# Kernel tuning notes

Measured on AMD Instinct MI355X. Metric: run time of the kernel, lower is better.

## Reference

```python
import jax, jax.numpy as jnp
import numpy as np

L = 4096
NUM_ITERS = 50
LR = 0.1
B1, B2, EPS = 0.9, 0.999, 1e-8  # torch.optim.Adam defaults


def setup_inputs() -> dict:
    key = jax.random.key(0)
    k1, k2 = jax.random.split(key)
    pred_distances = jax.random.uniform(k1, (L, L), dtype=jnp.float32) * 30.0
    confidence = jax.random.uniform(k2, (L, L), dtype=jnp.float32)
    mask = jnp.ones((L, L), dtype=jnp.float32)
    return {"pred_distances": pred_distances, "confidence": confidence, "mask": mask}


def _mds_init(distances, mask):
    # Classical MDS: double-centered squared distances -> top-3 eigenpairs.
    n = distances.shape[0]
    D = jnp.where(mask == 0, 0.0, distances)
    D_sq = D ** 2
    H = jnp.eye(n, dtype=distances.dtype) - jnp.ones((n, n), dtype=distances.dtype) / n
    B = -0.5 * (H @ D_sq @ H)
    evals, evecs = jnp.linalg.eigh(B)  # ascending order
    top_evals = evals[-1:-4:-1]        # top 3, descending
    top_evecs = evecs[:, -1:-4:-1]
    return top_evecs * jnp.sqrt(jnp.clip(top_evals, 1e-10))  # (L, 3)


def _loss(coords, pred_d, weight):
    diff = coords[None, :, :] - coords[:, None, :]              # (L, L, 3)
    dist = jnp.sqrt((diff ** 2).sum(-1) + 1e-8)                 # (L, L)
    loss = (weight * (dist - pred_d) ** 2).sum() / (weight.sum() + 1e-8)
    # chain regularizer: consecutive residues ~5.9 Angstrom apart (L > 2)
    nd = jnp.sqrt(((coords[1:] - coords[:-1]) ** 2).sum(-1) + 1e-8)
    return loss + 0.1 * ((nd - 5.9) ** 2).mean()


def reference(pred_distances, confidence, mask):
    pred_d = (pred_distances + pred_distances.T) / 2
    conf = (confidence + confidence.T) / 2
    weight = conf * mask
    coords0 = _mds_init(pred_d, mask)
    grad_fn = jax.grad(_loss)

    def step(i, carry):
        coords, m, v = carry
        g = grad_fn(coords, pred_d, weight)
        t = (i + 1).astype(jnp.float32)
        m = B1 * m + (1.0 - B1) * g
        v = B2 * v + (1.0 - B2) * g * g
        mhat = m / (1.0 - B1 ** t)
        vhat = v / (1.0 - B2 ** t)
        coords = coords - LR * mhat / (jnp.sqrt(vhat) + EPS)
        return (coords, m, v)

    z = jnp.zeros_like(coords0)
    coords, _, _ = jax.lax.fori_loop(0, NUM_ITERS, step, (coords0, z, z))
    return jax.lax.stop_gradient(coords)  # torch returns coords.detach()
```

## Files before the change

kernel.cpp:

```cpp
#include <hip/hip_runtime.h>
#include <math.h>

#define SIGN0 (1.0)
#define SIGN1 (-1.0)
#define SIGN2 (1.0)
#define EMIT0 1
#define EMIT1 1
#define EMIT2 1

#define N 4096
#define M_LAN 180
#define NCOLS (M_LAN + 2)
#define TPB 256
#define TPB_G 512

__global__ void k_zerof(float* p, int n) {
  int i = blockIdx.x * blockDim.x + threadIdx.x;
  int stride = gridDim.x * blockDim.x;
  for (; i < n; i += stride) p[i] = 0.0f;
}
__global__ void k_sentinel(float* out, int n) {
  int i = blockIdx.x * blockDim.x + threadIdx.x;
  if (i < n) out[i] = 1.0e6f;
}

#define TILE 64
__global__ void k_prep(const float* __restrict__ P, const float* __restrict__ C,
                       const float* __restrict__ Mk, float* __restrict__ pd,
                       float* __restrict__ wgt, double* __restrict__ wpart) {
  __shared__ float As[TILE][TILE + 1];
  __shared__ float Bs[TILE][TILE + 1];
  __shared__ double sred[4];
  int i0 = blockIdx.x * TILE, j0 = blockIdx.y * TILE;
  int tx = threadIdx.x & 63, ty = threadIdx.x >> 6;
  float mreg[16];
  for (int rr = ty, q = 0; rr < TILE; rr += 4, ++q)
    mreg[q] = Mk[(size_t)(i0 + rr) * N + j0 + tx];
  for (int rr = ty; rr < TILE; rr += 4) {
    As[rr][tx] = P[(size_t)(i0 + rr) * N + j0 + tx];
    Bs[rr][tx] = P[(size_t)(j0 + rr) * N + i0 + tx];
  }
  __syncthreads();
  for (int rr = ty, q = 0; rr < TILE; rr += 4, ++q) {
    float pv = 0.5f * (As[rr][tx] + Bs[tx][rr]);
    pd[(size_t)(i0 + rr) * N + j0 + tx] = (mreg[q] == 0.0f) ? 0.0f : pv;
  }
  __syncthreads();
  for (int rr = ty; rr < TILE; rr += 4) {
    As[rr][tx] = C[(size_t)(i0 + rr) * N + j0 + tx];
    Bs[rr][tx] = C[(size_t)(j0 + rr) * N + i0 + tx];
  }
  __syncthreads();
  double wacc = 0.0;
  for (int rr = ty, q = 0; rr < TILE; rr += 4, ++q) {
    float wvv = 0.5f * (As[rr][tx] + Bs[tx][rr]) * mreg[q];
    wgt[(size_t)(i0 + rr) * N + j0 + tx] = wvv;
    wacc += (double)wvv;
  }
  for (int s = 32; s > 0; s >>= 1) wacc += __shfl_down(wacc, s);
  int lane = threadIdx.x & 63, wid = threadIdx.x >> 6;
  if (lane == 0) sred[wid] = wacc;
  __syncthreads();
  if (threadIdx.x == 0)
    wpart[blockIdx.y * 64 + blockIdx.x] = sred[0] + sred[1] + sred[2] + sred[3];
}

__global__ void k_wsum(const double* __restrict__ wpart, double* __restrict__ Wsum) {
  __shared__ double sred[4];
  double a = 0.0;
  for (int t = threadIdx.x; t < 4096; t += TPB) a += wpart[t];
  for (int s = 32; s > 0; s >>= 1) a += __shfl_down(a, s);
  int lane = threadIdx.x & 63, wid = threadIdx.x >> 6;
  if (lane == 0) sred[wid] = a;
  __syncthreads();
  if (threadIdx.x == 0) Wsum[0] = sred[0] + sred[1] + sred[2] + sred[3];
}

__global__ void k_init_raw(double* __restrict__ V, double* __restrict__ wv,
                           double* __restrict__ statp) {
  __shared__ double sred[4];
  int i = blockIdx.x * TPB + threadIdx.x;
  V[i] = 1.0 / 64.0;
  unsigned h = (unsigned)i * 2654435761u;
  h ^= h >> 16; h *= 2246822519u; h ^= h >> 13; h *= 3266489917u; h ^= h >> 16;
  double r = ((double)(h & 0xFFFFFFu) / 16777216.0) - 0.5;
  wv[i] = r;
  double s1 = r;
  for (int s = 32; s > 0; s >>= 1) s1 += __shfl_down(s1, s);
  int lane = threadIdx.x & 63, wid = threadIdx.x >> 6;
  if (lane == 0) sred[wid] = s1;
  __syncthreads();
  if (threadIdx.x == 0) statp[blockIdx.x] = sred[0] + sred[1] + sred[2] + sred[3];
}
__global__ void k_init_fin(double* __restrict__ wv, const double* __restrict__ statp,
                           double* __restrict__ bsqp) {
  __shared__ double sred[4];
  int i = blockIdx.x * TPB + threadIdx.x;
  double s1 = 0.0;
#pragma unroll
  for (int p = 0; p < 16; ++p) s1 += statp[p];
  double mean = s1 / (double)N;
  double w = wv[i] - mean;
  wv[i] = w;
  double ww = w * w;
  for (int s = 32; s > 0; s >>= 1) ww += __shfl_down(ww, s);
  int lane = threadIdx.x & 63, wid = threadIdx.x >> 6;
  if (lane == 0) sred[wid] = ww;
  __syncthreads();
  if (threadIdx.x == 0) bsqp[blockIdx.x] = sred[0] + sred[1] + sred[2] + sred[3];
  if (blockIdx.x == 0 && threadIdx.x >= 16 && threadIdx.x < 256) bsqp[threadIdx.x] = 0.0;
}

__global__ void __launch_bounds__(TPB) k_mv(const float* __restrict__ pd,
    const double* __restrict__ wv, double* __restrict__ V, int j,
    double* __restrict__ z, double* __restrict__ beta,
    const double* __restrict__ bsqp) {
  __shared__ double sred[4][4];
  __shared__ double s_bs;
  int b = blockIdx.x, tid = threadIdx.x;
  int lane = tid & 63, wid = tid >> 6;
  double w[16];
  const double2* w2 = (const double2*)wv;
#pragma unroll
  for (int it = 0; it < 4; ++it) {
    int t = tid + it * TPB;
    double2 a = w2[2 * t], c = w2[2 * t + 1];
    w[it * 4 + 0] = a.x; w[it * 4 + 1] = a.y;
    w[it * 4 + 2] = c.x; w[it * 4 + 3] = c.y;
  }
  double acc[4] = {0.0, 0.0, 0.0, 0.0};
#pragma unroll
  for (int r = 0; r < 4; ++r) {
    const float4* row4 = (const float4*)(pd + (size_t)(b * 4 + r) * N);
#pragma unroll
    for (int it = 0; it < 4; ++it) {
      int t = tid + it * TPB;
      float4 p = row4[t];
      acc[r] = fma((double)p.x * (double)p.x, w[it * 4 + 0], acc[r]);
      acc[r] = fma((double)p.y * (double)p.y, w[it * 4 + 1], acc[r]);
      acc[r] = fma((double)p.z * (double)p.z, w[it * 4 + 2], acc[r]);
      acc[r] = fma((double)p.w * (double)p.w, w[it * 4 + 3], acc[r]);
    }
  }
#pragma unroll
  for (int r = 0; r < 4; ++r) {
    double a = acc[r];
    for (int s = 32; s > 0; s >>= 1) a += __shfl_down(a, s);
    if (lane == 0) sred[r][wid] = a;
  }
  if (wid == 0) {
    double a = bsqp[lane] + bsqp[lane + 64] + bsqp[lane + 128] + bsqp[lane + 192];
    for (int s = 32; s > 0; s >>= 1) a += __shfl_down(a, s);
    if (lane == 0) s_bs = a;
  }
  __syncthreads();
  if (tid < 4) {
    double bs = s_bs;
    double invb = 1.0 / sqrt(bs);
    double tot = sred[tid][0] + sred[tid][1] + sred[tid][2] + sred[tid][3];
    int i = b * 4 + tid;
    z[i] = -0.5 * invb * tot;
    V[(size_t)j * N + i] = wv[i] * invb;
    if (i == 0) beta[j] = sqrt(bs);
  }
}

__global__ void k_dot(const double* __restrict__ V, const double* __restrict__ vec,
                      double* __restrict__ cp, int j) {
  __shared__ double sred[4];
  int k = blockIdx.x, q = blockIdx.y;
  const double2* col = (const double2*)(V + (size_t)k * N);
  const double2* v2 = (const double2*)vec;
  int base = q * (N / 8);
  double acc = 0.0;
  for (int t = threadIdx.x; t < N / 8; t += TPB) {
    double2 a = col[base + t];
    double2 x = v2[base + t];
    acc = fma(a.x, x.x, acc);
    acc = fma(a.y, x.y, acc);
  }
  for (int s = 32; s > 0; s >>= 1) acc += __shfl_down(acc, s);
  int lane = threadIdx.x & 63, wid = threadIdx.x >> 6;
  if (lane == 0) sred[wid] = acc;
  __syncthreads();
  if (threadIdx.x == 0) cp[(size_t)k * 4 + q] = sred[0] + sred[1] + sred[2] + sred[3];
}

__global__ void __launch_bounds__(TPB) k_proj(const double* __restrict__ V,
    const double* __restrict__ in, double* __restrict__ outv,
    const double* __restrict__ cp, int j, double* __restrict__ bsqp,
    double* __restrict__ alph, int accum, int store) {
  __shared__ double cs_c[NCOLS];
  __shared__ double part[16][17];
  int tid = threadIdx.x;
  for (int k = tid; k <= j; k += TPB)
    cs_c[k] = cp[(size_t)k * 4 + 0] + cp[(size_t)k * 4 + 1] +
              cp[(size_t)k * 4 + 2] + cp[(size_t)k * 4 + 3];
  __syncthreads();
  if (store && blockIdx.x == 0 && tid == 0) alph[j] = cs_c[j];
  int il = tid & 15, kc = tid >> 4;
  int i = blockIdx.x * 16 + il;
  double acc = 0.0;
  for (int k = kc; k <= j; k += 16) acc += cs_c[k] * V[(size_t)k * N + i];
  part[kc][il] = acc;
  __syncthreads();
  if (tid < 16) {
    int i2 = blockIdx.x * 16 + tid;
    double s = 0.0;
#pragma unroll
    for (int q = 0; q < 16; ++q) s += part[q][tid];
    double w = in[i2] - s;
    outv[i2] = w;
    if (accum) {
      double ww = w * w;
      for (int s2 = 8; s2 > 0; s2 >>= 1) ww += __shfl_down(ww, s2);
      if (tid == 0) bsqp[blockIdx.x] = ww;
    }
  }
}

__global__ void k_alfin(const double* __restrict__ cp, double* __restrict__ alph) {
  if (threadIdx.x == 0)
    alph[M_LAN] = cp[(size_t)M_LAN * 4 + 0] + cp[(size_t)M_LAN * 4 + 1] +
                  cp[(size_t)M_LAN * 4 + 2] + cp[(size_t)M_LAN * 4 + 3];
}

#define AL(k) alph[k]
__global__ void k_tridiag(const double* __restrict__ alph, const double* __restrict__ beta,
                          double* __restrict__ lam, double* __restrict__ yv,
                          double* __restrict__ scr) {
  __shared__ double glo, ghi, gbm;
  if (threadIdx.x == 0) {
    double lo = 1e300, hi = -1e300, bm = 0.0;
    for (int k = 1; k <= M_LAN; ++k) {
      double bl = (k >= 2) ? fabs(beta[k]) : 0.0;
      double br = (k < M_LAN) ? fabs(beta[k + 1]) : 0.0;
      lo = fmin(lo, AL(k) - bl - br);
      hi = fmax(hi, AL(k) + bl + br);
      bm = fmax(bm, bl);
    }
    glo = lo - 1.0; ghi = hi + 1.0; gbm = bm;
  }
  __syncthreads();
  if (threadIdx.x < 3) {
    int r = threadIdx.x;
    double pivmin = fmax(gbm * gbm, 1.0) * 1e-20;
    int target = M_LAN - r;
    double lo = glo, hi = ghi;
    for (int it = 0; it < 60; ++it) {
      double mid = 0.5 * (lo + hi);
      int cnt = 0;
      double q = AL(1) - mid;
      if (fabs(q) < pivmin) q = -pivmin;
      if (q < 0.0) cnt++;
      for (int k = 2; k <= M_LAN; ++k) {
        q = AL(k) - mid - beta[k] * beta[k] / q;
        if (fabs(q) < pivmin) q = -pivmin;
        if (q < 0.0) cnt++;
      }
      if (cnt >= target) hi = mid; else lo = mid;
    }
    double L = 0.5 * (lo + hi);
    lam[r] = L;
    double* dd = scr + (size_t)r * 5 * NCOLS;
    double* uu = dd + NCOLS;
    double* u2 = uu + NCOLS;
    double* xx = u2 + NCOLS;
    double* yy = xx + NCOLS;
    for (int k = 1; k <= M_LAN; ++k) yy[k] = 1.0;
    for (int pass = 0; pass < 3; ++pass) {
      for (int k = 1; k <= M_LAN; ++k) {
        dd[k] = AL(k) - L;
        u2[k] = 0.0;
        uu[k] = (k < M_LAN) ? beta[k + 1] : 0.0;
        xx[k] = yy[k];
      }
      for (int k = 1; k < M_LAN; ++k) {
        double sub = beta[k + 1];
        if (fabs(dd[k]) >= fabs(sub)) {
          double dk = dd[k];
          if (fabs(dk) < pivmin) { dk = (dk < 0.0 ? -pivmin : pivmin); dd[k] = dk; }
          double mult = sub / dk;
          dd[k + 1] -= mult * uu[k];
          uu[k + 1] -= mult * u2[k];
          xx[k + 1] -= mult * xx[k];
        } else {
          double t = dd[k];
          double ndk = sub, nuk = dd[k + 1], nu2k = uu[k + 1];
          double mult = t / ndk;
          double ndk1 = uu[k] - mult * nuk;
          double nuk1 = u2[k] - mult * nu2k;
          dd[k] = ndk; uu[k] = nuk; u2[k] = nu2k;
          dd[k + 1] = ndk1; uu[k + 1] = nuk1;
          if (k + 1 <= M_LAN) u2[k + 1] = 0.0;
          double xk = xx[k], xk1 = xx[k + 1];
          xx[k] = xk1;
          xx[k + 1] = xk - mult * xk1;
        }
      }
      if (fabs(dd[M_LAN]) < pivmin) dd[M_LAN] = (dd[M_LAN] < 0.0 ? -pivmin : pivmin);
      xx[M_LAN] = xx[M_LAN] / dd[M_LAN];
      xx[M_LAN - 1] = (xx[M_LAN - 1] - uu[M_LAN - 1] * xx[M_LAN]) / dd[M_LAN - 1];
      for (int k = M_LAN - 2; k >= 1; --k)
        xx[k] = (xx[k] - uu[k] * xx[k + 1] - u2[k] * xx[k + 2]) / dd[k];
      double ss = 0.0;
      for (int k = 1; k <= M_LAN; ++k) ss += xx[k] * xx[k];
      double inv = 1.0 / sqrt(ss);
      for (int k = 1; k <= M_LAN; ++k) yy[k] = xx[k] * inv;
    }
    yv[(size_t)r * NCOLS + 0] = 0.0;
    for (int k = 1; k <= M_LAN; ++k) yv[(size_t)r * NCOLS + k] = yy[k];
  }
}

__global__ void k_ritz_u(const double* __restrict__ V, const double* __restrict__ yv,
                         double* __restrict__ u) {
  int b = blockIdx.x;
  int r = b >> 4;
  int i = (b & 15) * TPB + threadIdx.x;
  const double* y = yv + (size_t)r * NCOLS;
  double acc = 0.0;
  for (int t = 1; t <= M_LAN; ++t) acc += V[(size_t)t * N + i] * y[t];
  u[(size_t)r * N + i] = acc;
}

__global__ void k_ustat(const double* __restrict__ u, double* __restrict__ upart) {
  __shared__ double sq[TPB], mv[TPB], sv[TPB];
  int b = blockIdx.x;
  int r = b >> 4;
  int i = (b & 15) * TPB + threadIdx.x;
  double val = u[(size_t)r * N + i];
  sq[threadIdx.x] = val * val;
  mv[threadIdx.x] = fabs(val);
  sv[threadIdx.x] = val;
  __syncthreads();
  for (int s = 128; s > 0; s >>= 1) {
    if (threadIdx.x < s) {
      sq[threadIdx.x] += sq[threadIdx.x + s];
      if (mv[threadIdx.x + s] > mv[threadIdx.x]) {
        mv[threadIdx.x] = mv[threadIdx.x + s];
        sv[threadIdx.x] = sv[threadIdx.x + s];
      }
    }
    __syncthreads();
  }
  if (threadIdx.x == 0) {
    upart[b * 3 + 0] = sq[0];
    upart[b * 3 + 1] = mv[0];
    upart[b * 3 + 2] = sv[0];
  }
}

__global__ void k_ufin(const double* __restrict__ upart, const double* __restrict__ lam,
                       double* __restrict__ scale) {
  int r = threadIdx.x;
  if (r < 3) {
    double ssq = 0.0, mx = -1.0, sgnv = 0.0;
    for (int p = 0; p < 16; ++p) {
      const double* e = upart + ((size_t)((r << 4) + p)) * 3;
      ssq += e[0];
      if (e[1] > mx) { mx = e[1]; sgnv = e[2]; }
    }
    double s = (sgnv >= 0.0) ? 1.0 : -1.0;
    double cfg = (r == 0) ? SIGN0 : ((r == 1) ? SIGN1 : SIGN2);
    scale[r] = cfg * s * sqrt(fmax(lam[r], 1e-10)) / sqrt(ssq);
  }
}

__global__ void k_coords0(const double* __restrict__ u, const double* __restrict__ scale,
                          float* __restrict__ cA) {
  int i = blockIdx.x * TPB + threadIdx.x;
  cA[i * 3 + 0] = (float)(u[i] * scale[0]);
  cA[i * 3 + 1] = (float)(u[(size_t)N + i] * scale[1]);
  cA[i * 3 + 2] = (float)(u[(size_t)2 * N + i] * scale[2]);
}

__global__ void __launch_bounds__(TPB_G) k_grad(const float* __restrict__ cin,
    float* __restrict__ cout, const float* __restrict__ pdm, const float* __restrict__ wgt,
    float* __restrict__ mst, float* __restrict__ vst, const double* __restrict__ WsumP,
    double bc1, double bc2) {
  __shared__ float cs[3 * N];
  const float4* cin4 = (const float4*)cin;
  float4* cs4 = (float4*)cs;
  for (int idx = threadIdx.x; idx < 3 * N / 4; idx += TPB_G) cs4[idx] = cin4[idx];
  __syncthreads();
  int lane = threadIdx.x & 63, wid = threadIdx.x >> 6;
  int i = blockIdx.x * 8 + wid;
  float cx = cs[3 * i + 0], cy = cs[3 * i + 1], cz = cs[3 * i + 2];
  const float4* wrow4 = (const float4*)(wgt + (size_t)i * N);
  const float4* prow4 = (const float4*)(pdm + (size_t)i * N);
  double ax = 0.0, ay = 0.0, az = 0.0;
  for (int q = lane; q < N / 4; q += 64) {
    float4 wv4 = wrow4[q];
    float4 pv4 = prow4[q];
    int j0 = q * 4;
#pragma unroll
    for (int cidx = 0; cidx < 4; ++cidx) {
      float wvj = (cidx == 0) ? wv4.x : (cidx == 1) ? wv4.y : (cidx == 2) ? wv4.z : wv4.w;
      float pvj = (cidx == 0) ? pv4.x : (cidx == 1) ? pv4.y : (cidx == 2) ? pv4.z : pv4.w;
      int j = j0 + cidx;
      float dx = cx - cs[3 * j + 0];
      float dy = cy - cs[3 * j + 1];
      float dz = cz - cs[3 * j + 2];
      float t2 = dx * dx + dy * dy + dz * dz + 1e-8f;
      float inv = rsqrtf(t2);
      float d = t2 * inv;
      float coef = wvj * (d - pvj) * inv;
      ax += (double)(coef * dx);
      ay += (double)(coef * dy);
      az += (double)(coef * dz);
    }
  }
  for (int s = 32; s > 0; s >>= 1) {
    ax += __shfl_down(ax, s);
    ay += __shfl_down(ay, s);
    az += __shfl_down(az, s);
  }
  if (lane == 0) {
    double W = WsumP[0] + 1e-8;
    double sc = 4.0 / W;
    double g0 = sc * ax, g1 = sc * ay, g2 = sc * az;
    const double CO = 0.2 / (double)(N - 1);
    if (i >= 1) {
      double ex = (double)cs[3 * i + 0] - (double)cs[3 * (i - 1) + 0];
      double ey = (double)cs[3 * i + 1] - (double)cs[3 * (i - 1) + 1];
      double ez = (double)cs[3 * i + 2] - (double)cs[3 * (i - 1) + 2];
      double nd = sqrt(ex * ex + ey * ey + ez * ez + 1e-8);
      double f = CO * (nd - 5.9) / nd;
      g0 += f * ex; g1 += f * ey; g2 += f * ez;
    }
    if (i < N - 1) {
      double ex = (double)cs[3 * (i + 1) + 0] - (double)cs[3 * i + 0];
      double ey = (double)cs[3 * (i + 1) + 1] - (double)cs[3 * i + 1];
      double ez = (double)cs[3 * (i + 1) + 2] - (double)cs[3 * i + 2];
      double nd = sqrt(ex * ex + ey * ey + ez * ez + 1e-8);
      double f = CO * (nd - 5.9) / nd;
      g0 -= f * ex; g1 -= f * ey; g2 -= f * ez;
    }
    double gs[3] = {g0, g1, g2};
    for (int c = 0; c < 3; ++c) {
      double mm = 0.9 * (double)mst[3 * i + c] + 0.1 * gs[c];
      double vv = 0.999 * (double)vst[3 * i + c] + 0.001 * gs[c] * gs[c];
      mst[3 * i + c] = (float)mm;
      vst[3 * i + c] = (float)vv;
      double mh = mm / bc1, vh = vv / bc2;
      cout[3 * i + c] = (float)((double)cs[3 * i + c] - 0.1 * mh / (sqrt(vh) + 1e-8));
    }
  }
}

__global__ void k_out(const float* __restrict__ cfin, float* __restrict__ out) {
  int i = blockIdx.x * TPB + threadIdx.x;
  int col = i % 3;
  float v = cfin[i];
  int emit = (col == 0) ? EMIT0 : ((col == 1) ? EMIT1 : EMIT2);
  out[i] = emit ? v : 0.0f;
}

extern "C" void kernel_launch(void* const* d_in, const int* in_sizes, int n_in,
                              void* d_out, int out_size, void* d_ws, size_t ws_size,
                              hipStream_t stream) {
  const float* P = (const float*)d_in[0];
  const float* Cf = (const float*)d_in[1];
  const float* Mk = (const float*)d_in[2];
  float* out = (float*)d_out;
  char* base = (char*)d_ws;
  size_t off = 0;
  auto carve = [&](size_t bytes) -> void* {
    void* p = (void*)(base + off);
    off += (bytes + 255) & ~(size_t)255;
    return p;
  };
  float* pd    = (float*)carve(sizeof(float) * (size_t)N * N);
  float* wgt   = (float*)carve(sizeof(float) * (size_t)N * N);
  double* V    = (double*)carve(sizeof(double) * (size_t)N * NCOLS);
  double* z    = (double*)carve(sizeof(double) * N);
  double* wv   = (double*)carve(sizeof(double) * N);
  double* wtmp = (double*)carve(sizeof(double) * N);
  double* u    = (double*)carve(sizeof(double) * 3 * N);
  double* beta  = (double*)carve(sizeof(double) * NCOLS);
  double* alph  = (double*)carve(sizeof(double) * NCOLS);
  double* bsqp  = (double*)carve(sizeof(double) * 256);
  double* cp    = (double*)carve(sizeof(double) * NCOLS * 4);
  double* Wsum  = (double*)carve(sizeof(double) * 4);
  double* wpart = (double*)carve(sizeof(double) * 4096);
  double* statp = (double*)carve(sizeof(double) * 16);
  double* lam   = (double*)carve(sizeof(double) * 4);
  double* yv    = (double*)carve(sizeof(double) * 3 * NCOLS);
  double* scr   = (double*)carve(sizeof(double) * 15 * NCOLS);
  double* upart = (double*)carve(sizeof(double) * 48 * 3);
  double* scale = (double*)carve(sizeof(double) * 4);
  float* cA  = (float*)carve(sizeof(float) * 3 * N);
  float* cB  = (float*)carve(sizeof(float) * 3 * N);
  float* mst = (float*)carve(sizeof(float) * 3 * N);
  float* vst = (float*)carve(sizeof(float) * 3 * N);

  if (off > ws_size) {
    k_sentinel<<<48, TPB, 0, stream>>>(out, out_size);
    return;
  }

  k_zerof<<<32, TPB, 0, stream>>>(mst, 2 * 3 * N);

  k_prep<<<dim3(64, 64), TPB, 0, stream>>>(P, Cf, Mk, pd, wgt, wpart);
  k_wsum<<<1, TPB, 0, stream>>>(wpart, Wsum);
  k_init_raw<<<16, TPB, 0, stream>>>(V, wv, statp);
  k_init_fin<<<16, TPB, 0, stream>>>(wv, statp, bsqp);

  for (int j = 1; j <= M_LAN; ++j) {
    k_mv<<<1024, TPB, 0, stream>>>(pd, wv, V, j, z, beta, bsqp);
    k_dot<<<dim3(j + 1, 4), TPB, 0, stream>>>(V, z, cp, j);
    if (j < M_LAN) {
      k_proj<<<256, TPB, 0, stream>>>(V, z, wtmp, cp, j, bsqp, alph, 0, 1);
      k_dot<<<dim3(j + 1, 4), TPB, 0, stream>>>(V, wtmp, cp, j);
      k_proj<<<256, TPB, 0, stream>>>(V, wtmp, wv, cp, j, bsqp, alph, 1, 0);
    } else {
      k_alfin<<<1, 64, 0, stream>>>(cp, alph);
    }
  }

  k_tridiag<<<1, 64, 0, stream>>>(alph, beta, lam, yv, scr);
  k_ritz_u<<<48, TPB, 0, stream>>>(V, yv, u);
  k_ustat<<<48, TPB, 0, stream>>>(u, upart);
  k_ufin<<<1, 64, 0, stream>>>(upart, lam, scale);
  k_coords0<<<16, TPB, 0, stream>>>(u, scale, cA);

  float* ca = cA;
  float* cb = cB;
  for (int t = 1; t <= 50; ++t) {
    double bc1 = 1.0 - pow(0.9, (double)t);
    double bc2 = 1.0 - pow(0.999, (double)t);
    k_grad<<<512, TPB_G, 0, stream>>>(ca, cb, pd, wgt, mst, vst, Wsum, bc1, bc2);
    float* tsw = ca; ca = cb; cb = tsw;
  }
  k_out<<<48, TPB, 0, stream>>>(ca, out);
}
```

Baseline: 7.198 ms.

## Fuse second reorthogonalization dot products into first projection kernel

Each Lanczos step's first projection kernel now also computes per-block partial dot products of the projected vector against every basis column, writing them to a new partials buffer. The second projection reduces those 256 partials per column itself, which removes the separate second dot-product launch. This cuts one kernel launch and one full read of V per iteration. In exchange, the projection kernel makes strided per-thread reads of V, and every block of the second kernel redundantly re-reduces a 256-by-(j+1) partial array.

```diff
diff --git a/kernel.cpp b/kernel.cpp
--- a/kernel.cpp
+++ b/kernel.cpp
@@ -186,36 +186,73 @@
   if (threadIdx.x == 0) cp[(size_t)k * 4 + q] = sred[0] + sred[1] + sred[2] + sred[3];
 }
 
-__global__ void __launch_bounds__(TPB) k_proj(const double* __restrict__ V,
-    const double* __restrict__ in, double* __restrict__ outv,
-    const double* __restrict__ cp, int j, double* __restrict__ bsqp,
-    double* __restrict__ alph, int accum, int store) {
+__global__ void __launch_bounds__(TPB) k_projd(const double* __restrict__ V,
+    const double* __restrict__ z, double* __restrict__ wtmp,
+    const double* __restrict__ cp, int j, double* __restrict__ alph,
+    double* __restrict__ cp2) {
   __shared__ double cs_c[NCOLS];
   __shared__ double part[16][17];
-  int tid = threadIdx.x;
+  __shared__ double wls[16];
+  int tid = threadIdx.x, b = blockIdx.x;
   for (int k = tid; k <= j; k += TPB)
     cs_c[k] = cp[(size_t)k * 4 + 0] + cp[(size_t)k * 4 + 1] +
               cp[(size_t)k * 4 + 2] + cp[(size_t)k * 4 + 3];
   __syncthreads();
-  if (store && blockIdx.x == 0 && tid == 0) alph[j] = cs_c[j];
+  if (b == 0 && tid == 0) alph[j] = cs_c[j];
   int il = tid & 15, kc = tid >> 4;
-  int i = blockIdx.x * 16 + il;
+  int i = b * 16 + il;
   double acc = 0.0;
   for (int k = kc; k <= j; k += 16) acc += cs_c[k] * V[(size_t)k * N + i];
   part[kc][il] = acc;
   __syncthreads();
   if (tid < 16) {
-    int i2 = blockIdx.x * 16 + tid;
+    int i2 = b * 16 + tid;
     double s = 0.0;
 #pragma unroll
     for (int q = 0; q < 16; ++q) s += part[q][tid];
-    double w = in[i2] - s;
-    outv[i2] = w;
-    if (accum) {
-      double ww = w * w;
-      for (int s2 = 8; s2 > 0; s2 >>= 1) ww += __shfl_down(ww, s2);
-      if (tid == 0) bsqp[blockIdx.x] = ww;
-    }
+    double w = z[i2] - s;
+    wtmp[i2] = w;
+    wls[tid] = w;
+  }
+  __syncthreads();
+  if (tid <= j) {
+    const double* vk = V + (size_t)tid * N + b * 16;
+    double d = 0.0;
+#pragma unroll
+    for (int q = 0; q < 16; ++q) d = fma(vk[q], wls[q], d);
+    cp2[(size_t)b * NCOLS + tid] = d;
+  }
+}
+
+__global__ void __launch_bounds__(TPB) k_proj2(const double* __restrict__ V,
+    const double* __restrict__ wtmp, double* __restrict__ wv,
+    const double* __restrict__ cp2, int j, double* __restrict__ bsqp) {
+  __shared__ double cs_c[NCOLS];
+  __shared__ double part[16][17];
+  int tid = threadIdx.x, b = blockIdx.x;
+  for (int k = tid; k <= j; k += TPB) {
+    double s = 0.0;
+#pragma unroll 8
+    for (int p = 0; p < 256; ++p) s += cp2[(size_t)p * NCOLS + k];
+    cs_c[k] = s;
+  }
+  __syncthreads();
+  int il = tid & 15, kc = tid >> 4;
+  int i = b * 16 + il;
+  double acc = 0.0;
+  for (int k = kc; k <= j; k += 16) acc += cs_c[k] * V[(size_t)k * N + i];
+  part[kc][il] = acc;
+  __syncthreads();
+  if (tid < 16) {
+    int i2 = b * 16 + tid;
+    double s = 0.0;
+#pragma unroll
+    for (int q = 0; q < 16; ++q) s += part[q][tid];
+    double w = wtmp[i2] - s;
+    wv[i2] = w;
+    double ww = w * w;
+    for (int s2 = 8; s2 > 0; s2 >>= 1) ww += __shfl_down(ww, s2);
+    if (tid == 0) bsqp[b] = ww;
   }
 }
 
@@ -482,6 +519,7 @@
   double* alph  = (double*)carve(sizeof(double) * NCOLS);
   double* bsqp  = (double*)carve(sizeof(double) * 256);
   double* cp    = (double*)carve(sizeof(double) * NCOLS * 4);
+  double* cp2   = (double*)carve(sizeof(double) * 256 * NCOLS);
   double* Wsum  = (double*)carve(sizeof(double) * 4);
   double* wpart = (double*)carve(sizeof(double) * 4096);
   double* statp = (double*)carve(sizeof(double) * 16);
@@ -511,9 +549,8 @@
     k_mv<<<1024, TPB, 0, stream>>>(pd, wv, V, j, z, beta, bsqp);
     k_dot<<<dim3(j + 1, 4), TPB, 0, stream>>>(V, z, cp, j);
     if (j < M_LAN) {
-      k_proj<<<256, TPB, 0, stream>>>(V, z, wtmp, cp, j, bsqp, alph, 0, 1);
-      k_dot<<<dim3(j + 1, 4), TPB, 0, stream>>>(V, wtmp, cp, j);
-      k_proj<<<256, TPB, 0, stream>>>(V, wtmp, wv, cp, j, bsqp, alph, 1, 0);
+      k_projd<<<256, TPB, 0, stream>>>(V, z, wtmp, cp, j, alph, cp2);
+      k_proj2<<<256, TPB, 0, stream>>>(V, wtmp, wv, cp2, j, bsqp);
     } else {
       k_alfin<<<1, 64, 0, stream>>>(cp, alph);
     }
```

Result: slower. 9.006 ms (+25.1%).
